# Performance work log

Measured on AMD Instinct MI355X. Metric: run time of the kernel, lower is better.

Reference implementation:

```python
import math
import jax, jax.numpy as jnp
import numpy as np

D_MODEL = 1024
N_HEADS = 16
D_K = D_MODEL // N_HEADS
B, T = 2, 2048


def setup_inputs() -> dict:
    key = jax.random.key(0)
    kx, kq, kk, kv, ko = jax.random.split(key, 5)
    x = jax.random.normal(kx, (B, T, D_MODEL), dtype=jnp.float32)
    # causal mask, 1 = keep, 0 = masked (broadcast over batch & heads)
    mask = jnp.tril(jnp.ones((T, T), dtype=jnp.int32))[None, None, :, :]
    s = 1.0 / math.sqrt(D_MODEL)
    # nn.Linear stores weight as [out, in]; y = x @ W.T
    W_q = jax.random.normal(kq, (D_MODEL, D_MODEL), dtype=jnp.float32) * s
    W_k = jax.random.normal(kk, (D_MODEL, D_MODEL), dtype=jnp.float32) * s
    W_v = jax.random.normal(kv, (D_MODEL, D_MODEL), dtype=jnp.float32) * s
    W_o = jax.random.normal(ko, (D_MODEL, D_MODEL), dtype=jnp.float32) * s
    return {"x": x, "mask": mask, "W_q": W_q, "W_k": W_k, "W_v": W_v, "W_o": W_o}


def _split_heads(y):
    # [B,T,D] -> [B,H,T,d_k]
    b, t, _ = y.shape
    return y.reshape(b, t, N_HEADS, D_K).transpose(0, 2, 1, 3)


def reference(x, mask, W_q, W_k, W_v, W_o):
    Q = _split_heads(x @ W_q.T)
    K = _split_heads(x @ W_k.T)
    V = _split_heads(x @ W_v.T)
    scores = jnp.einsum("bhqd,bhkd->bhqk", Q, K) / math.sqrt(D_K)
    scores = jnp.where(mask == 0, -jnp.inf, scores)
    attn = jax.nn.softmax(scores, axis=-1)
    out = jnp.einsum("bhqk,bhkd->bhqd", attn, V)
    out = out.transpose(0, 2, 1, 3).reshape(x.shape[0], x.shape[1], D_MODEL)
    return out @ W_o.T
```

## Files before the change

### kernel.cpp

```cpp
#include <hip/hip_runtime.h>

typedef __attribute__((ext_vector_type(8))) short short8;
typedef __attribute__((ext_vector_type(4))) float f32x4;
typedef __attribute__((ext_vector_type(16))) float f32x16;
typedef __attribute__((ext_vector_type(4))) unsigned short u16x4;
typedef __attribute__((ext_vector_type(4))) unsigned int u32x4;

#define T_SEQ   2048
#define NHEADS  16
#define DHEAD   64
#define DMODEL  1024
#define NBATCH  2
#define MROWS   (NBATCH * T_SEQ)

__device__ __forceinline__ unsigned short f2bf(float f) {
    unsigned int u = __float_as_uint(f);
    u += 0x7fffu + ((u >> 16) & 1u);
    return (unsigned short)(u >> 16);
}

__device__ __forceinline__ unsigned int cvtpk(float lo, float hi) {
    unsigned int r;
    asm("v_cvt_pk_bf16_f32 %0, %1, %2" : "=v"(r) : "v"(lo), "v"(hi));
    return r;
}

__device__ __forceinline__ void pl32(int a, int b, int& r0, int& r1) {
    auto r = __builtin_amdgcn_permlane32_swap(a, b, false, false);
    r0 = r[0]; r1 = r[1];
}

__device__ __forceinline__ void gld_lds16(const unsigned short* g, unsigned short* l) {
    __builtin_amdgcn_global_load_lds(
        (const __attribute__((address_space(1))) void*)g,
        (__attribute__((address_space(3))) void*)l, 16, 0, 0);
}

#define N8X (MROWS * DMODEL / 8)
#define N8W (DMODEL * DMODEL / 8)
__global__ __launch_bounds__(256) void k_convert_all(const float* __restrict__ x,
                                                     const float* __restrict__ w0,
                                                     const float* __restrict__ w1,
                                                     const float* __restrict__ w2,
                                                     const float* __restrict__ w3,
                                                     unsigned short* __restrict__ xbf,
                                                     unsigned short* __restrict__ wbf) {
    int i = blockIdx.x * blockDim.x + threadIdx.x;
    const float* src;
    unsigned short* dst;
    if (i < N8X) {
        src = x + (size_t)i * 8;
        dst = xbf + (size_t)i * 8;
    } else {
        int j = i - N8X;
        int which = j >> 17;
        const float* w = (which == 0) ? w0 : (which == 1) ? w1 : (which == 2) ? w2 : w3;
        src = w + (size_t)(j & (N8W - 1)) * 8;
        dst = wbf + (size_t)j * 8;
    }
    const float4* p = (const float4*)src;
    float4 a = p[0], b = p[1];
    short8 r;
    r[0] = (short)f2bf(a.x); r[1] = (short)f2bf(a.y);
    r[2] = (short)f2bf(a.z); r[3] = (short)f2bf(a.w);
    r[4] = (short)f2bf(b.x); r[5] = (short)f2bf(b.y);
    r[6] = (short)f2bf(b.z); r[7] = (short)f2bf(b.w);
    *(short8*)dst = r;
}

template <int MODE>
__global__ __launch_bounds__(256) void k_gemm_st(const unsigned short* __restrict__ A,
                                                 const unsigned short* __restrict__ Wm,
                                                 float* __restrict__ outF,
                                                 unsigned short* __restrict__ outQ,
                                                 unsigned short* __restrict__ outK,
                                                 unsigned short* __restrict__ outV) {
    __shared__ __align__(16) unsigned short smA[2][128 * 32];
    __shared__ __align__(16) unsigned short smB[2][128 * 32];
    const int tid  = threadIdx.x;
    const int lane = tid & 63;
    const int w    = tid >> 6;
    const int lr   = lane & 15;
    const int lg   = lane >> 4;
    const int m0   = blockIdx.y * 128;
    const int n0   = blockIdx.x * 128;
    const int wm   = (w >> 1) * 64;
    const int wn   = (w & 1) * 64;

    const int srow = w * 32 + (lane >> 2);
    const int scol = (lane & 3) * 8;
    const unsigned short* gA0 = A  + (size_t)(m0 + srow) * DMODEL + scol;
    const unsigned short* gB0 = Wm + (size_t)(n0 + srow) * DMODEL + scol;
    const int lo = w * 1024;

    f32x4 acc[4][4];
#pragma unroll
    for (int i = 0; i < 4; i++)
#pragma unroll
        for (int j = 0; j < 4; j++) acc[i][j] = (f32x4){0.f, 0.f, 0.f, 0.f};

#define STAGE(K0, BUF) do {                                            \
        gld_lds16(gA0 + (K0),               smA[BUF] + lo);            \
        gld_lds16(gA0 + 16 * DMODEL + (K0), smA[BUF] + lo + 16 * 32);  \
        gld_lds16(gB0 + (K0),               smB[BUF] + lo);            \
        gld_lds16(gB0 + 16 * DMODEL + (K0), smB[BUF] + lo + 16 * 32);  \
    } while (0)

#define FRAG_READ(BUF)                                                           \
        short8 af[4], bfr[4];                                                    \
        {                                                                        \
            const unsigned short* sA = smA[BUF];                                 \
            const unsigned short* sB = smB[BUF];                                 \
            _Pragma("unroll")                                                    \
            for (int i = 0; i < 4; i++)                                          \
                af[i] = *(const short8*)&sA[(wm + 16 * i + lr) * 32 + lg * 8];   \
            _Pragma("unroll")                                                    \
            for (int j = 0; j < 4; j++)                                          \
                bfr[j] = *(const short8*)&sB[(wn + 16 * j + lr) * 32 + lg * 8];  \
        }

#define MFMA16()                                                                 \
        _Pragma("unroll")                                                        \
        for (int i = 0; i < 4; i++)                                              \
            _Pragma("unroll")                                                    \
            for (int j = 0; j < 4; j++)                                          \
                acc[i][j] = __builtin_amdgcn_mfma_f32_16x16x32_bf16(             \
                    af[i], bfr[j], acc[i][j], 0, 0, 0);

    STAGE(0, 0);
    STAGE(32, 1);

    for (int t = 0; t < 30; ++t) {
        asm volatile("s_waitcnt vmcnt(4)" ::: "memory");
        __builtin_amdgcn_s_barrier();
        FRAG_READ(t & 1)
        asm volatile("s_waitcnt lgkmcnt(0)" ::: "memory");
        __builtin_amdgcn_sched_barrier(0);
        __builtin_amdgcn_s_barrier();
        STAGE((t + 2) * 32, t & 1);
        MFMA16()
    }
    {
        asm volatile("s_waitcnt vmcnt(4)" ::: "memory");
        __builtin_amdgcn_s_barrier();
        FRAG_READ(0)
        MFMA16()
    }
    {
        asm volatile("s_waitcnt vmcnt(0)" ::: "memory");
        __builtin_amdgcn_s_barrier();
        FRAG_READ(1)
        MFMA16()
    }
#undef STAGE
#undef FRAG_READ
#undef MFMA16

    if (MODE == 0) {
#pragma unroll
        for (int i = 0; i < 4; i++)
#pragma unroll
            for (int j = 0; j < 4; j++) {
                int n = n0 + wn + 16 * j + lr;
#pragma unroll
                for (int r = 0; r < 4; r++) {
                    int mm = m0 + wm + 16 * i + lg * 4 + r;
                    outF[(size_t)mm * DMODEL + n] = acc[i][j][r];
                }
            }
    } else {
        const int which = n0 >> 10;
        const int nb = n0 & 1023;
        const float QS = 0.18033688f;
#pragma unroll
        for (int i = 0; i < 4; i++)
#pragma unroll
            for (int j = 0; j < 4; j++) {
                int nloc = nb + wn + 16 * j + lr;
                int h = nloc >> 6, d = nloc & 63;
                int mb = m0 + wm + 16 * i + lg * 4;
                int b = mb >> 11, t = mb & (T_SEQ - 1);
                size_t base = (size_t)(b * NHEADS + h) * T_SEQ * DHEAD;
                if (which == 2) {
                    int off = ((((t >> 6) * 2 + (d >> 5)) * 4 + ((t >> 4) & 3)) * 64
                               + ((t >> 3) & 1) * 32 + (d & 31)) * 8 + (t & 7);
                    u16x4 pk;
#pragma unroll
                    for (int r = 0; r < 4; r++) pk[r] = f2bf(acc[i][j][r]);
                    *(u16x4*)(outV + base + off) = pk;
                } else {
                    unsigned short* dst = (which == 0) ? outQ : outK;
                    const float sc = (which == 0) ? QS : 1.0f;
                    int off = (((t >> 5) * 4 + (d >> 4)) * 64 + (d & 8) * 4 + (t & 31)) * 8 + (d & 7);
#pragma unroll
                    for (int r = 0; r < 4; r++)
                        dst[base + off + r * 8] = f2bf(acc[i][j][r] * sc);
                }
            }
    }
}

__global__ __launch_bounds__(256) void k_gemm_o(const unsigned short* __restrict__ A,
                                                const unsigned short* __restrict__ Wm,
                                                float* __restrict__ outF) {
    __shared__ __align__(16) unsigned short smA[2][64 * 32];
    __shared__ __align__(16) unsigned short smB[2][64 * 32];
    const int tid  = threadIdx.x;
    const int lane = tid & 63;
    const int w    = tid >> 6;
    const int lr   = lane & 15;
    const int lg   = lane >> 4;
    const int m0   = blockIdx.y * 64;
    const int n0   = blockIdx.x * 64;
    const int wm   = (w >> 1) * 32;
    const int wn   = (w & 1) * 32;

    const int sr   = w * 16 + (lane >> 2);
    const int scol = (lane & 3) * 8;
    const unsigned short* gA0 = A  + (size_t)(m0 + sr) * DMODEL + scol;
    const unsigned short* gB0 = Wm + (size_t)(n0 + sr) * DMODEL + scol;
    const int lo = w * 512;

    f32x4 acc[2][2];
#pragma unroll
    for (int i = 0; i < 2; i++)
#pragma unroll
        for (int j = 0; j < 2; j++) acc[i][j] = (f32x4){0.f, 0.f, 0.f, 0.f};

#define STAGE(K0, BUF) do {                          \
        gld_lds16(gA0 + (K0), smA[BUF] + lo);        \
        gld_lds16(gB0 + (K0), smB[BUF] + lo);        \
    } while (0)

#define FRAG_READ(BUF)                                                           \
        short8 af[2], bfr[2];                                                    \
        {                                                                        \
            const unsigned short* sA = smA[BUF];                                 \
            const unsigned short* sB = smB[BUF];                                 \
            _Pragma("unroll")                                                    \
            for (int i = 0; i < 2; i++)                                          \
                af[i] = *(const short8*)&sA[(wm + 16 * i + lr) * 32 + lg * 8];   \
            _Pragma("unroll")                                                    \
            for (int j = 0; j < 2; j++)                                          \
                bfr[j] = *(const short8*)&sB[(wn + 16 * j + lr) * 32 + lg * 8];  \
        }

#define MFMA4()                                                                  \
        _Pragma("unroll")                                                        \
        for (int i = 0; i < 2; i++)                                              \
            _Pragma("unroll")                                                    \
            for (int j = 0; j < 2; j++)                                          \
                acc[i][j] = __builtin_amdgcn_mfma_f32_16x16x32_bf16(             \
                    af[i], bfr[j], acc[i][j], 0, 0, 0);

    STAGE(0, 0);
    STAGE(32, 1);

    for (int t = 0; t < 30; ++t) {
        asm volatile("s_waitcnt vmcnt(2)" ::: "memory");
        __builtin_amdgcn_s_barrier();
        FRAG_READ(t & 1)
        asm volatile("s_waitcnt lgkmcnt(0)" ::: "memory");
        __builtin_amdgcn_sched_barrier(0);
        __builtin_amdgcn_s_barrier();
        STAGE((t + 2) * 32, t & 1);
        MFMA4()
    }
    {
        asm volatile("s_waitcnt vmcnt(2)" ::: "memory");
        __builtin_amdgcn_s_barrier();
        FRAG_READ(0)
        MFMA4()
    }
    {
        asm volatile("s_waitcnt vmcnt(0)" ::: "memory");
        __builtin_amdgcn_s_barrier();
        FRAG_READ(1)
        MFMA4()
    }
#undef STAGE
#undef FRAG_READ
#undef MFMA4

#pragma unroll
    for (int i = 0; i < 2; i++)
#pragma unroll
        for (int j = 0; j < 2; j++) {
            int n = n0 + wn + 16 * j + lr;
#pragma unroll
            for (int r = 0; r < 4; r++) {
                int mm = m0 + wm + 16 * i + lg * 4 + r;
                outF[(size_t)mm * DMODEL + n] = acc[i][j][r];
            }
        }
}

__global__ __launch_bounds__(256) void k_attn(const unsigned short* __restrict__ Q,
                                              const unsigned short* __restrict__ K,
                                              const unsigned short* __restrict__ Vt,
                                              unsigned short* __restrict__ O) {
    __shared__ float Msm[3][64][33];
    const int tid  = threadIdx.x;
    const int lane = tid & 63;
    const int wv   = tid >> 6;
    const int l31  = lane & 31;
    const int hi   = lane >> 5;

    const int flat = blockIdx.x;
    const int xc   = flat & 7;
    const int rest = flat >> 3;
    const int hh   = rest >> 5;
    const int pr   = rest & 31;
    const int bh   = xc * 4 + hh;

    const size_t baseQK = (size_t)bh * T_SEQ * DHEAD;
    const unsigned short* Qb = Q  + baseQK;
    const unsigned short* Kb = K  + baseQK;
    const unsigned short* Vb = Vt + baseQK;

    for (int phase = 0; phase < 2; ++phase) {
        const int qt = phase ? pr : (63 - pr);
        const int q0 = qt * 32;
        const int ntiles = (qt >> 1) + 1;
        const int qlane = q0 + l31;

        short8 qf[4];
#pragma unroll
        for (int dt = 0; dt < 4; dt++)
            qf[dt] = *(const short8*)(Qb + ((size_t)(qt * 4 + dt) * 64 + lane) * 8);

        f32x16 oa0, oa1;
#pragma unroll
        for (int r = 0; r < 16; r++) { oa0[r] = 0.f; oa1[r] = 0.f; }
        float l = 0.f;

        const unsigned short* pK = Kb + (size_t)wv * 4096 + (size_t)lane * 8;
        const unsigned short* pV = Vb + (size_t)wv * 4096 + (size_t)lane * 8;

        for (int tix = wv; tix < ntiles; tix += 4) {
            f32x16 s0, s1;
#pragma unroll
            for (int r = 0; r < 16; r++) { s0[r] = 0.f; s1[r] = 0.f; }
            {
                short8 kf0[4], kf1[4];
#pragma unroll
                for (int kt = 0; kt < 4; kt++) {
                    kf0[kt] = *(const short8*)(pK + kt * 512);
                    kf1[kt] = *(const short8*)(pK + 2048 + kt * 512);
                }
                __builtin_amdgcn_s_setprio(1);
#pragma unroll
                for (int dt = 0; dt < 4; dt++)
                    s0 = __builtin_amdgcn_mfma_f32_32x32x16_bf16(kf0[dt], qf[dt], s0, 0, 0, 0);
#pragma unroll
                for (int dt = 0; dt < 4; dt++)
                    s1 = __builtin_amdgcn_mfma_f32_32x32x16_bf16(kf1[dt], qf[dt], s1, 0, 0, 0);
                __builtin_amdgcn_s_setprio(0);
            }

            short8 vf0[4], vf1[4];
#pragma unroll
            for (int kt = 0; kt < 4; kt++) {
                vf0[kt] = *(const short8*)(pV + kt * 512);
                vf1[kt] = *(const short8*)(pV + 2048 + kt * 512);
            }
            pK += 16384;
            pV += 16384;

            if (tix == ntiles - 1) {
                const int thr = qlane - tix * 64;
#pragma unroll
                for (int r = 0; r < 16; r++) {
                    const int koff = (r & 3) + 8 * (r >> 2) + 4 * hi;
                    if (koff > thr)      s0[r] = -1e30f;
                    if (koff + 32 > thr) s1[r] = -1e30f;
                }
            }

#pragma unroll
            for (int r = 0; r < 16; r++) {
                s0[r] = __builtin_amdgcn_exp2f(s0[r]);
                s1[r] = __builtin_amdgcn_exp2f(s1[r]);
            }
            float u8[8];
#pragma unroll
            for (int i = 0; i < 8; i++)
                u8[i] = (s0[i] + s0[i + 8]) + (s1[i] + s1[i + 8]);
            float u4a = u8[0] + u8[4], u4b = u8[1] + u8[5];
            float u4c = u8[2] + u8[6], u4d = u8[3] + u8[7];
            float sum = (u4a + u4b) + (u4c + u4d);
            {
                int r0, r1;
                pl32(__float_as_int(sum), __float_as_int(sum), r0, r1);
                sum = __int_as_float(r0) + __int_as_float(r1);
            }
            l += sum;

            unsigned int ow0[8], ow1[8];
#pragma unroll
            for (int q_ = 0; q_ < 8; q_++) {
                ow0[q_] = cvtpk(s0[2 * q_], s0[2 * q_ + 1]);
                ow1[q_] = cvtpk(s1[2 * q_], s1[2 * q_ + 1]);
            }

            __builtin_amdgcn_s_setprio(1);
#define PV_STEP(KT, OW, J) do {                                                  \
        int ra0, ra1, rb0, rb1;                                                  \
        pl32((int)OW[J],     (int)OW[J + 2], ra0, ra1);                          \
        pl32((int)OW[J + 1], (int)OW[J + 3], rb0, rb1);                          \
        u32x4 wvv;                                                               \
        wvv[0] = (unsigned)ra0; wvv[1] = (unsigned)rb0;                          \
        wvv[2] = (unsigned)ra1; wvv[3] = (unsigned)rb1;                          \
        short8 pf = __builtin_bit_cast(short8, wvv);                             \
        oa0 = __builtin_amdgcn_mfma_f32_32x32x16_bf16(vf0[KT], pf, oa0, 0, 0, 0);\
        oa1 = __builtin_amdgcn_mfma_f32_32x32x16_bf16(vf1[KT], pf, oa1, 0, 0, 0);\
    } while (0)

            PV_STEP(0, ow0, 0);
            PV_STEP(1, ow0, 4);
            PV_STEP(2, ow1, 0);
            PV_STEP(3, ow1, 4);
#undef PV_STEP
            __builtin_amdgcn_s_setprio(0);
        }

        const int merger = phase;
        if (phase == 1) __syncthreads();
        if (wv != merger) {
            const int slot = wv - (wv > merger ? 1 : 0);
#pragma unroll
            for (int r = 0; r < 16; r++) {
                Msm[slot][lane][r]      = oa0[r];
                Msm[slot][lane][16 + r] = oa1[r];
            }
            Msm[slot][lane][32] = l;
        }
        __syncthreads();
        if (wv == merger) {
            float lt = l;
#pragma unroll
            for (int s = 0; s < 3; s++) lt += Msm[s][lane][32];
            const float inv = 1.0f / lt;
            const int b = bh >> 4, h = bh & 15;
            unsigned short* orow = O + ((size_t)(b * T_SEQ + qlane)) * DMODEL + h * DHEAD;
#pragma unroll
            for (int rg = 0; rg < 4; rg++) {
                u16x4 pk0, pk1;
#pragma unroll
                for (int jj = 0; jj < 4; jj++) {
                    const int idx = 4 * rg + jj;
                    float v0 = oa0[idx];
                    float v1 = oa1[idx];
#pragma unroll
                    for (int s = 0; s < 3; s++) {
                        v0 += Msm[s][lane][idx];
                        v1 += Msm[s][lane][16 + idx];
                    }
                    pk0[jj] = f2bf(v0 * inv);
                    pk1[jj] = f2bf(v1 * inv);
                }
                *(u16x4*)(orow + 4 * hi + 8 * rg) = pk0;
                *(u16x4*)(orow + 32 + 4 * hi + 8 * rg) = pk1;
            }
        }
    }
}

extern "C" void kernel_launch(void* const* d_in, const int* in_sizes, int n_in,
                              void* d_out, int out_size, void* d_ws, size_t ws_size,
                              hipStream_t stream) {
    const float* x  = (const float*)d_in[0];
    const float* Wq = (const float*)d_in[2];
    const float* Wk = (const float*)d_in[3];
    const float* Wv = (const float*)d_in[4];
    const float* Wo = (const float*)d_in[5];

    unsigned short* wsu = (unsigned short*)d_ws;
    const size_t WELE = (size_t)DMODEL * DMODEL;
    unsigned short* Wo_bf = wsu + 3 * WELE;
    unsigned short* x_bf  = wsu + 4 * WELE;
    unsigned short* Qp    = wsu + 8 * WELE;
    unsigned short* Kp    = wsu + 12 * WELE;
    unsigned short* Vp    = wsu + 16 * WELE;
    if (ws_size < 20 * WELE * sizeof(unsigned short)) return;

    const int nAll = N8X + 4 * N8W;
    k_convert_all<<<dim3(nAll / 256), 256, 0, stream>>>(x, Wq, Wk, Wv, Wo, x_bf, wsu);

    k_gemm_st<1><<<dim3(3 * DMODEL / 128, MROWS / 128), 256, 0, stream>>>(
        x_bf, wsu, nullptr, Qp, Kp, Vp);

    k_attn<<<dim3(1024), 256, 0, stream>>>(Qp, Kp, Vp, x_bf);

    k_gemm_o<<<dim3(DMODEL / 64, MROWS / 64), 256, 0, stream>>>(
        x_bf, Wo_bf, (float*)d_out);
}
```

Before: 100.7 us.

## Fuse fp32-to-bf16 conversion of x into QKV GEMM A-tile loads

The activation x is no longer converted to bf16 in a separate pass. The QKV GEMM now stages fp32 A tiles straight into LDS using an XOR-swizzled layout and converts them to bf16 with v_cvt_pk_bf16_f32 while reading fragments. The B tile reads also gain a swizzle to reduce LDS bank conflicts. This removes a full read and write of x through a bf16 buffer, but doubles the LDS footprint and global load count for A and adds conversion ALU work inside the GEMM loop.

```diff
diff --git a/kernel.cpp b/kernel.cpp
--- a/kernel.cpp
+++ b/kernel.cpp
@@ -30,34 +30,23 @@
     r0 = r[0]; r1 = r[1];
 }
 
-__device__ __forceinline__ void gld_lds16(const unsigned short* g, unsigned short* l) {
+__device__ __forceinline__ void gld_lds16(const void* g, void* l) {
     __builtin_amdgcn_global_load_lds(
         (const __attribute__((address_space(1))) void*)g,
         (__attribute__((address_space(3))) void*)l, 16, 0, 0);
 }
 
-#define N8X (MROWS * DMODEL / 8)
 #define N8W (DMODEL * DMODEL / 8)
-__global__ __launch_bounds__(256) void k_convert_all(const float* __restrict__ x,
-                                                     const float* __restrict__ w0,
-                                                     const float* __restrict__ w1,
-                                                     const float* __restrict__ w2,
-                                                     const float* __restrict__ w3,
-                                                     unsigned short* __restrict__ xbf,
-                                                     unsigned short* __restrict__ wbf) {
+__global__ __launch_bounds__(256) void k_convert_w(const float* __restrict__ w0,
+                                                   const float* __restrict__ w1,
+                                                   const float* __restrict__ w2,
+                                                   const float* __restrict__ w3,
+                                                   unsigned short* __restrict__ wbf) {
     int i = blockIdx.x * blockDim.x + threadIdx.x;
-    const float* src;
-    unsigned short* dst;
-    if (i < N8X) {
-        src = x + (size_t)i * 8;
-        dst = xbf + (size_t)i * 8;
-    } else {
-        int j = i - N8X;
-        int which = j >> 17;
-        const float* w = (which == 0) ? w0 : (which == 1) ? w1 : (which == 2) ? w2 : w3;
-        src = w + (size_t)(j & (N8W - 1)) * 8;
-        dst = wbf + (size_t)j * 8;
-    }
+    int which = i >> 17;
+    const float* w = (which == 0) ? w0 : (which == 1) ? w1 : (which == 2) ? w2 : w3;
+    const float* src = w + (size_t)(i & (N8W - 1)) * 8;
+    unsigned short* dst = wbf + (size_t)i * 8;
     const float4* p = (const float4*)src;
     float4 a = p[0], b = p[1];
     short8 r;
@@ -68,14 +57,12 @@
     *(short8*)dst = r;
 }
 
-template <int MODE>
-__global__ __launch_bounds__(256) void k_gemm_st(const unsigned short* __restrict__ A,
-                                                 const unsigned short* __restrict__ Wm,
-                                                 float* __restrict__ outF,
-                                                 unsigned short* __restrict__ outQ,
-                                                 unsigned short* __restrict__ outK,
-                                                 unsigned short* __restrict__ outV) {
-    __shared__ __align__(16) unsigned short smA[2][128 * 32];
+__global__ __launch_bounds__(256) void k_gemm_qkv(const float* __restrict__ A,
+                                                  const unsigned short* __restrict__ Wm,
+                                                  unsigned short* __restrict__ outQ,
+                                                  unsigned short* __restrict__ outK,
+                                                  unsigned short* __restrict__ outV) {
+    __shared__ __align__(16) float          smA[2][128 * 32];
     __shared__ __align__(16) unsigned short smB[2][128 * 32];
     const int tid  = threadIdx.x;
     const int lane = tid & 63;
@@ -87,11 +74,18 @@
     const int wm   = (w >> 1) * 64;
     const int wn   = (w & 1) * 64;
 
-    const int srow = w * 32 + (lane >> 2);
-    const int scol = (lane & 3) * 8;
-    const unsigned short* gA0 = A  + (size_t)(m0 + srow) * DMODEL + scol;
-    const unsigned short* gB0 = Wm + (size_t)(n0 + srow) * DMODEL + scol;
-    const int lo = w * 1024;
+    const int srA  = w * 32 + (lane >> 3);
+    const int scA  = ((lane & 7) ^ (lane >> 3)) * 4;
+    const float* gA0 = A + (size_t)(m0 + srA) * DMODEL + scA;
+    const int srB  = w * 32 + (lane >> 2);
+    const int scB  = ((lane & 3) ^ ((lane >> 2) & 3)) * 8;
+    const unsigned short* gB0 = Wm + (size_t)(n0 + srB) * DMODEL + scB;
+    const int loA = w * 1024;
+    const int loB = w * 1024;
+
+    const int sA1 = ((2 * lg)     ^ (lr & 7)) * 4;
+    const int sA2 = ((2 * lg + 1) ^ (lr & 7)) * 4;
+    const int sB1 = (lg ^ (lr & 3)) * 8;
 
     f32x4 acc[4][4];
 #pragma unroll
@@ -99,24 +93,33 @@
 #pragma unroll
         for (int j = 0; j < 4; j++) acc[i][j] = (f32x4){0.f, 0.f, 0.f, 0.f};
 
-#define STAGE(K0, BUF) do {                                            \
-        gld_lds16(gA0 + (K0),               smA[BUF] + lo);            \
-        gld_lds16(gA0 + 16 * DMODEL + (K0), smA[BUF] + lo + 16 * 32);  \
-        gld_lds16(gB0 + (K0),               smB[BUF] + lo);            \
-        gld_lds16(gB0 + 16 * DMODEL + (K0), smB[BUF] + lo + 16 * 32);  \
+#define STAGE(K0, BUF) do {                                              \
+        gld_lds16(gA0 + (K0),                smA[BUF] + loA);            \
+        gld_lds16(gA0 + 8  * DMODEL + (K0),  smA[BUF] + loA + 8  * 32);  \
+        gld_lds16(gA0 + 16 * DMODEL + (K0),  smA[BUF] + loA + 16 * 32);  \
+        gld_lds16(gA0 + 24 * DMODEL + (K0),  smA[BUF] + loA + 24 * 32);  \
+        gld_lds16(gB0 + (K0),                smB[BUF] + loB);            \
+        gld_lds16(gB0 + 16 * DMODEL + (K0),  smB[BUF] + loB + 16 * 32);  \
     } while (0)
 
 #define FRAG_READ(BUF)                                                           \
         short8 af[4], bfr[4];                                                    \
         {                                                                        \
-            const unsigned short* sA = smA[BUF];                                 \
+            const float* sA = smA[BUF];                                          \
             const unsigned short* sB = smB[BUF];                                 \
             _Pragma("unroll")                                                    \
-            for (int i = 0; i < 4; i++)                                          \
-                af[i] = *(const short8*)&sA[(wm + 16 * i + lr) * 32 + lg * 8];   \
+            for (int i = 0; i < 4; i++) {                                        \
+                const int ro = (wm + 16 * i + lr) * 32;                          \
+                f32x4 a0 = *(const f32x4*)&sA[ro + sA1];                         \
+                f32x4 a1 = *(const f32x4*)&sA[ro + sA2];                         \
+                u32x4 aw;                                                        \
+                aw[0] = cvtpk(a0[0], a0[1]); aw[1] = cvtpk(a0[2], a0[3]);        \
+                aw[2] = cvtpk(a1[0], a1[1]); aw[3] = cvtpk(a1[2], a1[3]);        \
+                af[i] = __builtin_bit_cast(short8, aw);                          \
+            }                                                                    \
             _Pragma("unroll")                                                    \
             for (int j = 0; j < 4; j++)                                          \
-                bfr[j] = *(const short8*)&sB[(wn + 16 * j + lr) * 32 + lg * 8];  \
+                bfr[j] = *(const short8*)&sB[(wn + 16 * j + lr) * 32 + sB1];     \
         }
 
 #define MFMA16()                                                                 \
@@ -131,7 +134,7 @@
     STAGE(32, 1);
 
     for (int t = 0; t < 30; ++t) {
-        asm volatile("s_waitcnt vmcnt(4)" ::: "memory");
+        asm volatile("s_waitcnt vmcnt(6)" ::: "memory");
         __builtin_amdgcn_s_barrier();
         FRAG_READ(t & 1)
         asm volatile("s_waitcnt lgkmcnt(0)" ::: "memory");
@@ -141,7 +144,7 @@
         MFMA16()
     }
     {
-        asm volatile("s_waitcnt vmcnt(4)" ::: "memory");
+        asm volatile("s_waitcnt vmcnt(6)" ::: "memory");
         __builtin_amdgcn_s_barrier();
         FRAG_READ(0)
         MFMA16()
@@ -156,19 +159,7 @@
 #undef FRAG_READ
 #undef MFMA16
 
-    if (MODE == 0) {
-#pragma unroll
-        for (int i = 0; i < 4; i++)
-#pragma unroll
-            for (int j = 0; j < 4; j++) {
-                int n = n0 + wn + 16 * j + lr;
-#pragma unroll
-                for (int r = 0; r < 4; r++) {
-                    int mm = m0 + wm + 16 * i + lg * 4 + r;
-                    outF[(size_t)mm * DMODEL + n] = acc[i][j][r];
-                }
-            }
-    } else {
+    {
         const int which = n0 >> 10;
         const int nb = n0 & 1023;
         const float QS = 0.18033688f;
@@ -484,11 +475,10 @@
     unsigned short* Vp    = wsu + 16 * WELE;
     if (ws_size < 20 * WELE * sizeof(unsigned short)) return;
 
-    const int nAll = N8X + 4 * N8W;
-    k_convert_all<<<dim3(nAll / 256), 256, 0, stream>>>(x, Wq, Wk, Wv, Wo, x_bf, wsu);
-
-    k_gemm_st<1><<<dim3(3 * DMODEL / 128, MROWS / 128), 256, 0, stream>>>(
-        x_bf, wsu, nullptr, Qp, Kp, Vp);
+    k_convert_w<<<dim3(4 * N8W / 256), 256, 0, stream>>>(Wq, Wk, Wv, Wo, wsu);
+
+    k_gemm_qkv<<<dim3(3 * DMODEL / 128, MROWS / 128), 256, 0, stream>>>(
+        x, wsu, Qp, Kp, Vp);
 
     k_attn<<<dim3(1024), 256, 0, stream>>>(Qp, Kp, Vp, x_bf);
 
```

After: 106.4 us. 5.6% more time.
